# Kernel tuning notes

Hardware: AMD Instinct MI355X
Metric: run time of the kernel (lower is better)

Reference implementation:

```python
import jax, jax.numpy as jnp
import numpy as np

WIN = 256   # win_size
H = 8       # n_heads
D = 256     # feature_dim
DFF = 1024
EPS = 1e-5


def _layer_norm(x, g, b):
    mu = jnp.mean(x, axis=-1, keepdims=True)
    var = jnp.mean((x - mu) ** 2, axis=-1, keepdims=True)
    return (x - mu) * jax.lax.rsqrt(var + EPS) * g + b


def setup_inputs() -> dict:
    key = jax.random.key(0)
    ks = jax.random.split(key, 10)
    B, S = 8, 8192
    s = 0.02
    return {
        "query_em": jax.random.normal(ks[0], (B, S, D), jnp.float32),
        "key_value_em": jax.random.normal(ks[1], (B, S, D), jnp.float32),
        "Wq": jax.random.normal(ks[2], (D, D), jnp.float32) * s,
        "bq": jnp.zeros((D,), jnp.float32),
        "Wk": jax.random.normal(ks[3], (D, D), jnp.float32) * s,
        "bk": jnp.zeros((D,), jnp.float32),
        "Wv": jax.random.normal(ks[4], (D, D), jnp.float32) * s,
        "bv": jnp.zeros((D,), jnp.float32),
        "Wo": jax.random.normal(ks[5], (D, D), jnp.float32) * s,
        "bo": jnp.zeros((D,), jnp.float32),
        "ln1_g": jnp.ones((D,), jnp.float32),
        "ln1_b": jnp.zeros((D,), jnp.float32),
        "W1": jax.random.normal(ks[6], (D, DFF), jnp.float32) * s,
        "b1": jnp.zeros((DFF,), jnp.float32),
        "W2": jax.random.normal(ks[7], (DFF, D), jnp.float32) * s,
        "b2": jnp.zeros((D,), jnp.float32),
        "ln2_g": jnp.ones((D,), jnp.float32),
        "ln2_b": jnp.zeros((D,), jnp.float32),
    }


def reference(query_em, key_value_em, Wq, bq, Wk, bk, Wv, bv, Wo, bo,
              ln1_g, ln1_b, W1, b1, W2, b2, ln2_g, ln2_b):
    B, S, _ = query_em.shape
    nw = S // WIN
    dh = D // H

    # window partition: (B, S, D) -> (B*nw, w, D)
    q_in = query_em.reshape(B * nw, WIN, D)
    kv_in = key_value_em.reshape(B * nw, WIN, D)

    # generate_masks: padding_len == 0 -> all-False (nw, B, w, w) mask,
    # extract the block-diagonal windows, apply per window.
    mask = jnp.zeros((nw, B, WIN, WIN), dtype=bool)
    # reorder to (B*nw, 1, w, w) to broadcast over heads
    mask_bw = jnp.transpose(mask, (1, 0, 2, 3)).reshape(B * nw, 1, WIN, WIN)

    # multi-head cross attention within each window
    Q = (q_in @ Wq + bq).reshape(B * nw, WIN, H, dh)
    K = (kv_in @ Wk + bk).reshape(B * nw, WIN, H, dh)
    V = (kv_in @ Wv + bv).reshape(B * nw, WIN, H, dh)

    scores = jnp.einsum("nqhd,nkhd->nhqk", Q, K) / jnp.sqrt(jnp.float32(dh))
    scores = jnp.where(mask_bw, jnp.finfo(scores.dtype).min, scores)
    attn = jax.nn.softmax(scores, axis=-1)
    ctx = jnp.einsum("nhqk,nkhd->nqhd", attn, V).reshape(B * nw, WIN, D)
    attn_out = ctx @ Wo + bo

    # post-norm transformer encoder layer: residual + LN, FFN + LN
    x = _layer_norm(q_in + attn_out, ln1_g, ln1_b)
    ff = jax.nn.relu(x @ W1 + b1) @ W2 + b2
    y = _layer_norm(x + ff, ln2_g, ln2_b)

    # window merge: (B*nw, w, D) -> (B, S, D); padding_len == 0 so no slice
    return y.reshape(B, S, D)
```

## Files before the change

### kernel.cpp

```cpp
#include <hip/hip_runtime.h>

#define DEV __device__ __forceinline__

typedef short short4v __attribute__((ext_vector_type(4)));
typedef short short8v __attribute__((ext_vector_type(8)));
typedef float float4v __attribute__((ext_vector_type(4)));
typedef unsigned short u16;

DEV unsigned short f2bf(float f) {
  unsigned u = __builtin_bit_cast(unsigned, f);
  u += 0x7fffu + ((u >> 16) & 1u);
  return (unsigned short)(u >> 16);
}
DEV float bf2f(unsigned short h) {
  unsigned u = ((unsigned)h) << 16;
  return __builtin_bit_cast(float, u);
}
DEV float4v mfma32(short8v a, short8v b, float4v c) {
  return __builtin_amdgcn_mfma_f32_16x16x32_bf16(a, b, c, 0, 0, 0);
}
DEV float4v mfma16(short4v a, short4v b, float4v c) {
  return __builtin_amdgcn_mfma_f32_16x16x16bf16_1k(a, b, c, 0, 0, 0);
}
DEV void async16(const void* g, void* l) {
  __builtin_amdgcn_global_load_lds(
      (const __attribute__((address_space(1))) unsigned*)g,
      (__attribute__((address_space(3))) unsigned*)l, 16, 0, 0);
}
DEV short4v cvt4(float4v v) {
  short4v r;
  r[0] = (short)f2bf(v[0]); r[1] = (short)f2bf(v[1]);
  r[2] = (short)f2bf(v[2]); r[3] = (short)f2bf(v[3]);
  return r;
}

__global__ __launch_bounds__(256)
void cvt_in(const float* __restrict__ q, const float* __restrict__ kv,
            u16* __restrict__ qb, u16* __restrict__ kvb) {
  const float* src = blockIdx.y ? kv : q;
  u16* dst = blockIdx.y ? kvb : qb;
  size_t i = ((size_t)blockIdx.x * 256 + threadIdx.x) * 8;
  float4v a = *(const float4v*)(src + i);
  float4v b = *(const float4v*)(src + i + 4);
  short8v o;
  o[0] = (short)f2bf(a[0]); o[1] = (short)f2bf(a[1]);
  o[2] = (short)f2bf(a[2]); o[3] = (short)f2bf(a[3]);
  o[4] = (short)f2bf(b[0]); o[5] = (short)f2bf(b[1]);
  o[6] = (short)f2bf(b[2]); o[7] = (short)f2bf(b[3]);
  *(short8v*)(dst + i) = o;
}

__global__ __launch_bounds__(256)
void cvt_wT(const float* Wq, const float* Wk, const float* Wv, const float* Wo,
            const float* W1, const float* W2,
            u16* Wqt, u16* Wkt, u16* Wvt, u16* Wot, u16* W1t, u16* W2t) {
  __shared__ float ld[64 * 69];
  const float* src; u16* dst; int R, C; bool permk = false;
  switch (blockIdx.y) {
    case 0: src = Wq; dst = Wqt; R = 256;  C = 256;  break;
    case 1: src = Wk; dst = Wkt; R = 256;  C = 256;  break;
    case 2: src = Wv; dst = Wvt; R = 256;  C = 256;  break;
    case 3: src = Wo; dst = Wot; R = 256;  C = 256;  break;
    case 4: src = W1; dst = W1t; R = 256;  C = 1024; break;
    default: src = W2; dst = W2t; R = 1024; C = 256; permk = true; break;
  }
  const int ntile = (R >> 6) * (C >> 6);
  if ((int)blockIdx.x >= ntile) return;
  const int tf = blockIdx.x % (R >> 6);
  const int tn = blockIdx.x / (R >> 6);
  const int r0 = tf << 6, c0 = tn << 6;
  const int tid = threadIdx.x;
  {
    int lr = tid >> 4, lc = (tid & 15) << 2;
    #pragma unroll
    for (int ps = 0; ps < 4; ++ps) {
      int r = ps * 16 + lr;
      float4v v = *(const float4v*)(src + (size_t)(r0 + r) * C + c0 + lc);
      #pragma unroll
      for (int e = 0; e < 4; ++e) ld[r * 69 + lc + e] = v[e];
    }
  }
  __syncthreads();
  {
    int p8 = (tid & 7) << 3;
    #pragma unroll
    for (int ps = 0; ps < 2; ++ps) {
      int n = ps * 32 + (tid >> 3);
      short8v o;
      #pragma unroll
      for (int e = 0; e < 8; ++e) {
        int p = p8 + e;
        int fl = p;
        if (permk) {
          int m = p & 31;
          fl = (p & 32) + 16 * ((m >> 2) & 1) + 4 * (m >> 3) + (m & 3);
        }
        o[e] = (short)f2bf(ld[fl * 69 + n]);
      }
      *(short8v*)(dst + (size_t)(c0 + n) * R + r0 + p8) = o;
    }
  }
}

template<bool RESID>
__global__ __launch_bounds__(256, 2)
void gemm128(const u16* __restrict__ A, const u16* __restrict__ Wt,
             const float* __restrict__ bias, const float* __restrict__ resid,
             u16* __restrict__ out, int M, int N, int K) {
  __shared__ alignas(16) char sm[32768];
  char* sa = sm;
  char* sb = sm + 16384;
  const int tid = threadIdx.x;
  const int w = tid >> 6, lane = tid & 63;
  const int ln15 = lane & 15, gq = lane >> 4;
  const int wr = w >> 1, wc = w & 1;
  const int m0 = blockIdx.x * 128, n0 = blockIdx.y * 128;
  const char* Ab = (const char*)A;
  const char* Wb = (const char*)Wt;
  const int Kb = K * 2;

  float4v acc[4][4] = {};
  const int nk = K >> 6;
  for (int kk = 0; kk < nk; ++kk) {
    #pragma unroll
    for (int p = 0; p < 4; ++p) {
      int L = p * 4096 + w * 1024 + lane * 16;
      int row = L >> 7, colb = L & 127;
      int sw = colb ^ ((row & 7) << 4);
      async16(Ab + (size_t)(m0 + row) * Kb + kk * 128 + sw, sa + p * 4096 + w * 1024);
      async16(Wb + (size_t)(n0 + row) * Kb + kk * 128 + sw, sb + p * 4096 + w * 1024);
    }
    __syncthreads();
    #pragma unroll
    for (int ks = 0; ks < 2; ++ks) {
      short8v af[4], bfr[4];
      #pragma unroll
      for (int mf = 0; mf < 4; ++mf) {
        int r = wr * 64 + mf * 16 + ln15;
        af[mf] = *(const short8v*)(sa + r * 128 + ((ks * 64 + gq * 16) ^ ((r & 7) << 4)));
      }
      #pragma unroll
      for (int nf = 0; nf < 4; ++nf) {
        int r = wc * 64 + nf * 16 + ln15;
        bfr[nf] = *(const short8v*)(sb + r * 128 + ((ks * 64 + gq * 16) ^ ((r & 7) << 4)));
      }
      #pragma unroll
      for (int mf = 0; mf < 4; ++mf)
        #pragma unroll
        for (int nf = 0; nf < 4; ++nf)
          acc[mf][nf] = mfma32(af[mf], bfr[nf], acc[mf][nf]);
    }
    __syncthreads();
  }
  #pragma unroll
  for (int nf = 0; nf < 4; ++nf) {
    int col = n0 + wc * 64 + nf * 16 + ln15;
    float bb = bias[col];
    #pragma unroll
    for (int mf = 0; mf < 4; ++mf) {
      int rb = m0 + wr * 64 + mf * 16 + 4 * gq;
      #pragma unroll
      for (int j = 0; j < 4; ++j) {
        size_t idx = (size_t)(rb + j) * N + col;
        float v = acc[mf][nf][j] + bb;
        if (RESID) v += resid[idx];
        out[idx] = f2bf(v);
      }
    }
  }
}

__global__ __launch_bounds__(256, 2)
void gemm_kv(const u16* __restrict__ A, const u16* __restrict__ Wt,
             const float* __restrict__ bk, const float* __restrict__ bv,
             u16* __restrict__ Kout, u16* __restrict__ Vout) {
  __shared__ alignas(16) char sm[32768];
  char* sa = sm;
  char* sb = sm + 16384;
  const int tid = threadIdx.x;
  const int w = tid >> 6, lane = tid & 63;
  const int ln15 = lane & 15, gq = lane >> 4;
  const int wr = w >> 1, wc = w & 1;
  const int m0 = blockIdx.x * 128, n0 = blockIdx.y * 128;
  const char* Ab = (const char*)A;
  const char* Wb = (const char*)Wt;

  float4v acc[4][4] = {};
  for (int kk = 0; kk < 4; ++kk) {
    #pragma unroll
    for (int p = 0; p < 4; ++p) {
      int L = p * 4096 + w * 1024 + lane * 16;
      int row = L >> 7, colb = L & 127;
      int sw = colb ^ ((row & 7) << 4);
      async16(Ab + (size_t)(m0 + row) * 512 + kk * 128 + sw, sa + p * 4096 + w * 1024);
      async16(Wb + (size_t)(n0 + row) * 512 + kk * 128 + sw, sb + p * 4096 + w * 1024);
    }
    __syncthreads();
    #pragma unroll
    for (int ks = 0; ks < 2; ++ks) {
      short8v af[4], bfr[4];
      #pragma unroll
      for (int mf = 0; mf < 4; ++mf) {
        int r = wr * 64 + mf * 16 + ln15;
        af[mf] = *(const short8v*)(sa + r * 128 + ((ks * 64 + gq * 16) ^ ((r & 7) << 4)));
      }
      #pragma unroll
      for (int nf = 0; nf < 4; ++nf) {
        int r = wc * 64 + nf * 16 + ln15;
        bfr[nf] = *(const short8v*)(sb + r * 128 + ((ks * 64 + gq * 16) ^ ((r & 7) << 4)));
      }
      #pragma unroll
      for (int mf = 0; mf < 4; ++mf)
        #pragma unroll
        for (int nf = 0; nf < 4; ++nf)
          acc[mf][nf] = mfma32(af[mf], bfr[nf], acc[mf][nf]);
    }
    __syncthreads();
  }
  #pragma unroll
  for (int nf = 0; nf < 4; ++nf) {
    int col = n0 + wc * 64 + nf * 16 + ln15;
    const bool isK = col < 256;
    const int c2 = isK ? col : col - 256;
    u16* outp = isK ? Kout : Vout;
    float bb = isK ? bk[c2] : bv[c2];
    #pragma unroll
    for (int mf = 0; mf < 4; ++mf) {
      int rb = m0 + wr * 64 + mf * 16 + 4 * gq;
      #pragma unroll
      for (int j = 0; j < 4; ++j)
        outp[(size_t)(rb + j) * 256 + c2] = f2bf(acc[mf][nf][j] + bb);
    }
  }
}

__global__ __launch_bounds__(256, 2)
void attn_kernel(const u16* __restrict__ Qg, const u16* __restrict__ Kg,
                 const u16* __restrict__ Vg, u16* __restrict__ ctx) {
  __shared__ alignas(16) char vs[256 * 80];
  const int bw = blockIdx.x;
  const int win = bw >> 4, head = (bw >> 1) & 7, qh = bw & 1;
  const int tid = threadIdx.x;
  const int w = tid >> 6, lane = tid & 63;
  const int ln15 = lane & 15, gq = lane >> 4;
  const int tok0 = win << 8;
  const int q0 = qh * 128 + w * 32;

  {
    const u16* src = Vg + (size_t)(tok0 + tid) * 256 + head * 32;
    char* dst = vs + tid * 80;
    #pragma unroll
    for (int i = 0; i < 4; ++i)
      *(short8v*)(dst + i * 16) = *(const short8v*)(src + i * 8);
  }

  short8v qf[2];
  #pragma unroll
  for (int qi = 0; qi < 2; ++qi)
    qf[qi] = *(const short8v*)(Qg + (size_t)(tok0 + q0 + qi * 16 + ln15) * 256 + head * 32 + gq * 8);

  float4v s[16][2];
  #pragma unroll
  for (int kf = 0; kf < 16; ++kf) {
    short8v kfr = *(const short8v*)(Kg + (size_t)(tok0 + kf * 16 + ln15) * 256 + head * 32 + gq * 8);
    float4v z = {0.f, 0.f, 0.f, 0.f};
    s[kf][0] = mfma32(kfr, qf[0], z);
    s[kf][1] = mfma32(kfr, qf[1], z);
  }
  __syncthreads();

  const float KSC = (float)(1.4426950408889634 / 5.656854249492381);
  float rs[2];
  #pragma unroll
  for (int qi = 0; qi < 2; ++qi) {
    float mx = -1e30f;
    #pragma unroll
    for (int kf = 0; kf < 16; ++kf)
      #pragma unroll
      for (int j = 0; j < 4; ++j) mx = fmaxf(mx, s[kf][qi][j]);
    mx = fmaxf(mx, __shfl_xor(mx, 16));
    mx = fmaxf(mx, __shfl_xor(mx, 32));
    float sum = 0.f;
    #pragma unroll
    for (int kf = 0; kf < 16; ++kf)
      #pragma unroll
      for (int j = 0; j < 4; ++j) {
        float p = exp2f((s[kf][qi][j] - mx) * KSC);
        s[kf][qi][j] = p;
        sum += p;
      }
    sum += __shfl_xor(sum, 16);
    sum += __shfl_xor(sum, 32);
    rs[qi] = 1.0f / sum;
  }

  float4v cacc[2][2] = {};
  #pragma unroll
  for (int ks = 0; ks < 16; ++ks) {
    short4v pb[2];
    pb[0] = cvt4(s[ks][0]);
    pb[1] = cvt4(s[ks][1]);
    #pragma unroll
    for (int df = 0; df < 2; ++df) {
      const char* vb = vs + (size_t)(16 * ks + 4 * gq) * 80 + (df * 16 + ln15) * 2;
      short4v va;
      va[0] = *(const short*)(vb);
      va[1] = *(const short*)(vb + 80);
      va[2] = *(const short*)(vb + 160);
      va[3] = *(const short*)(vb + 240);
      cacc[df][0] = mfma16(va, pb[0], cacc[df][0]);
      cacc[df][1] = mfma16(va, pb[1], cacc[df][1]);
    }
  }

  #pragma unroll
  for (int qi = 0; qi < 2; ++qi)
    #pragma unroll
    for (int df = 0; df < 2; ++df) {
      short4v o;
      #pragma unroll
      for (int j = 0; j < 4; ++j) o[j] = (short)f2bf(cacc[df][qi][j] * rs[qi]);
      *(short4v*)(ctx + (size_t)(tok0 + q0 + qi * 16 + ln15) * 256 + head * 32 + df * 16 + 4 * gq) = o;
    }
}

__global__ __launch_bounds__(256, 4)
void ln_rows(u16* __restrict__ x, const float* __restrict__ g, const float* __restrict__ b) {
  int row = blockIdx.x * 4 + (threadIdx.x >> 6);
  int lane = threadIdx.x & 63;
  u16* p = x + (size_t)row * 256 + lane * 4;
  short4v v = *(short4v*)p;
  float f[4];
  #pragma unroll
  for (int i = 0; i < 4; ++i) f[i] = bf2f((unsigned short)v[i]);
  float s = f[0] + f[1] + f[2] + f[3];
  float ss = f[0] * f[0] + f[1] * f[1] + f[2] * f[2] + f[3] * f[3];
  #pragma unroll
  for (int m = 1; m <= 32; m <<= 1) {
    s += __shfl_xor(s, m);
    ss += __shfl_xor(ss, m);
  }
  float mu = s * (1.f / 256.f);
  float var = ss * (1.f / 256.f) - mu * mu;
  float rstd = rsqrtf(var + 1e-5f);
  #pragma unroll
  for (int i = 0; i < 4; ++i) {
    int c = lane * 4 + i;
    float o = (f[i] - mu) * rstd * g[c] + b[c];
    v[i] = (short)f2bf(o);
  }
  *(short4v*)p = v;
}

__global__ __launch_bounds__(512, 2)
void ffn_v6(const u16* __restrict__ X, const u16* __restrict__ W1t,
            const u16* __restrict__ W2tp, const float* __restrict__ b1,
            const float* __restrict__ b2, const float* __restrict__ g2,
            const float* __restrict__ be2, float* __restrict__ out) {
  __shared__ alignas(16) char w1c[2][16384];
  __shared__ alignas(16) char w2c[2][20480];
  __shared__ alignas(16) float b1s[1024];
  const int tid = threadIdx.x;
  const int w = tid >> 6, lane = tid & 63;
  const int ln15 = lane & 15, gq = lane >> 4;
  const int m0 = blockIdx.x * 256;
  const int wrow0 = m0 + w * 32;

  b1s[tid] = b1[tid];
  b1s[tid + 512] = b1[tid + 512];

  short8v xr[2][8];
  #pragma unroll
  for (int ct = 0; ct < 2; ++ct)
    #pragma unroll
    for (int kc = 0; kc < 8; ++kc)
      xr[ct][kc] = *(const short8v*)(X + (size_t)(wrow0 + ct * 16 + ln15) * 256 + kc * 32 + gq * 8);

  float4v ff[2][16] = {};
  short8v w2r[2];

  const char* W1b = (const char*)W1t;
  const char* W2b = (const char*)W2tp;

  #define STAGE_W1(buf, c)                                                     \
    {                                                                          \
      _Pragma("unroll")                                                        \
      for (int p = 0; p < 2; ++p) {                                            \
        int L = p * 8192 + tid * 16;                                           \
        int r = L >> 9, colb = L & 511;                                        \
        async16(W1b + (size_t)((c) * 32 + r) * 512 + (colb ^ ((r & 7) << 4)),  \
                w1c[buf] + L);                                                 \
      }                                                                        \
    }
  #define LOAD_W2(c)                                                           \
    {                                                                          \
      _Pragma("unroll")                                                        \
      for (int p = 0; p < 2; ++p) {                                            \
        int idx = p * 8192 + tid * 16;                                         \
        int n = idx >> 6, off = idx & 63;                                      \
        w2r[p] = *(const short8v*)(W2b + (size_t)n * 2048 + (c) * 64 + off);   \
      }                                                                        \
    }
  #define WRITE_W2(buf)                                                        \
    {                                                                          \
      _Pragma("unroll")                                                        \
      for (int p = 0; p < 2; ++p) {                                            \
        int idx = p * 8192 + tid * 16;                                         \
        int n = idx >> 6, off = idx & 63;                                      \
        *(short8v*)(w2c[buf] + n * 80 + off) = w2r[p];                         \
      }                                                                        \
    }

  STAGE_W1(0, 0);
  LOAD_W2(0);
  WRITE_W2(0);
  __syncthreads();

  #pragma unroll 2
  for (int c = 0; c < 32; ++c) {
    const int buf = c & 1;
    if (c < 31) {
      STAGE_W1(buf ^ 1, c + 1);
      LOAD_W2(c + 1);
    }

    float4v g1[2][2] = {};
    #pragma unroll
    for (int kc = 0; kc < 8; ++kc) {
      #pragma unroll
      for (int ft = 0; ft < 2; ++ft) {
        int r = ft * 16 + ln15;
        short8v a = *(const short8v*)(w1c[buf] + r * 512 +
                                      ((kc * 64 + gq * 16) ^ ((r & 7) << 4)));
        g1[0][ft] = mfma32(a, xr[0][kc], g1[0][ft]);
        g1[1][ft] = mfma32(a, xr[1][kc], g1[1][ft]);
      }
    }
    short8v pa8[2];
    #pragma unroll
    for (int ft = 0; ft < 2; ++ft) {
      float4v bv4 = *(const float4v*)(b1s + c * 32 + ft * 16 + 4 * gq);
      #pragma unroll
      for (int ct = 0; ct < 2; ++ct)
        #pragma unroll
        for (int j = 0; j < 4; ++j) {
          float v = g1[ct][ft][j] + bv4[j];
          v = v > 0.f ? v : 0.f;
          pa8[ct][ft * 4 + j] = (short)f2bf(v);
        }
    }
    #pragma unroll
    for (int nt = 0; nt < 16; ++nt) {
      short8v wb = *(const short8v*)(w2c[buf] + (nt * 16 + ln15) * 80 + gq * 16);
      ff[0][nt] = mfma32(pa8[0], wb, ff[0][nt]);
      ff[1][nt] = mfma32(pa8[1], wb, ff[1][nt]);
    }

    if (c < 31) WRITE_W2(buf ^ 1);
    __syncthreads();
  }

  #pragma unroll
  for (int ct = 0; ct < 2; ++ct)
    #pragma unroll
    for (int j = 0; j < 4; ++j) {
      int r2 = wrow0 + ct * 16 + 4 * gq + j;
      float sum = 0.f, sq = 0.f;
      float vv[16];
      #pragma unroll
      for (int nt = 0; nt < 16; ++nt) {
        int col = nt * 16 + ln15;
        float xv = bf2f(X[(size_t)r2 * 256 + col]);
        float v = ff[ct][nt][j] + b2[col] + xv;
        vv[nt] = v;
        sum += v;
        sq += v * v;
      }
      #pragma unroll
      for (int m = 1; m <= 8; m <<= 1) {
        sum += __shfl_xor(sum, m);
        sq += __shfl_xor(sq, m);
      }
      float mu = sum * (1.f / 256.f);
      float var = sq * (1.f / 256.f) - mu * mu;
      float rstd = rsqrtf(var + 1e-5f);
      #pragma unroll
      for (int nt = 0; nt < 16; ++nt) {
        int col = nt * 16 + ln15;
        out[(size_t)r2 * 256 + col] = (vv[nt] - mu) * rstd * g2[col] + be2[col];
      }
    }
  #undef STAGE_W1
  #undef LOAD_W2
  #undef WRITE_W2
}

extern "C" void kernel_launch(void* const* d_in, const int* in_sizes, int n_in,
                              void* d_out, int out_size, void* d_ws, size_t ws_size,
                              hipStream_t stream) {
  (void)in_sizes; (void)n_in; (void)out_size;
  const float* query = (const float*)d_in[0];
  const float* kv    = (const float*)d_in[1];
  const float* Wqm = (const float*)d_in[2];  const float* bq = (const float*)d_in[3];
  const float* Wkm = (const float*)d_in[4];  const float* bk = (const float*)d_in[5];
  const float* Wvm = (const float*)d_in[6];  const float* bv = (const float*)d_in[7];
  const float* Wom = (const float*)d_in[8];  const float* bo = (const float*)d_in[9];
  const float* ln1g = (const float*)d_in[10]; const float* ln1b = (const float*)d_in[11];
  const float* W1m = (const float*)d_in[12]; const float* b1 = (const float*)d_in[13];
  const float* W2m = (const float*)d_in[14]; const float* b2 = (const float*)d_in[15];
  const float* ln2g = (const float*)d_in[16]; const float* ln2b = (const float*)d_in[17];
  float* out = (float*)d_out;

  char* ws = (char*)d_ws;
  const size_t MB = 1ull << 20;
  if (ws_size < 130 * MB) return;

  u16* qbf  = (u16*)(ws);
  u16* kvbf = (u16*)(ws + 32 * MB);
  u16* Vw   = (u16*)(ws);
  u16* ctxw = (u16*)(ws + 32 * MB);
  u16* Qw   = (u16*)(ws + 64 * MB);
  u16* xw   = (u16*)(ws + 64 * MB);
  u16* Kw   = (u16*)(ws + 96 * MB);
  char* wb = ws + 128 * MB;
  u16* Wqt = (u16*)(wb);
  u16* Wkt = (u16*)(wb + 131072);
  u16* Wvt = (u16*)(wb + 262144);
  u16* Wot = (u16*)(wb + 393216);
  u16* W1t = (u16*)(wb + 524288);
  u16* W2t = (u16*)(wb + 1048576);

  cvt_in<<<dim3(8192, 2), 256, 0, stream>>>(query, kv, qbf, kvbf);
  cvt_wT<<<dim3(64, 6), 256, 0, stream>>>(Wqm, Wkm, Wvm, Wom, W1m, W2m,
                                          Wqt, Wkt, Wvt, Wot, W1t, W2t);
  gemm128<false><<<dim3(512, 2), 256, 0, stream>>>(qbf,  Wqt, bq, nullptr, Qw, 65536, 256, 256);
  gemm_kv<<<dim3(512, 4), 256, 0, stream>>>(kvbf, Wkt, bk, bv, Kw, Vw);
  attn_kernel<<<dim3(4096), 256, 0, stream>>>(Qw, Kw, Vw, ctxw);
  gemm128<true><<<dim3(512, 2), 256, 0, stream>>>(ctxw, Wot, bo, query, xw, 65536, 256, 256);
  ln_rows<<<dim3(16384), 256, 0, stream>>>(xw, ln1g, ln1b);
  ffn_v6<<<dim3(256), 512, 0, stream>>>(xw, W1t, W2t, b1, b2, ln2g, ln2b, out);
}
```

Measured before the change: 346.3 us.

## Use head-major Q/K/V/ctx layout and one block per window-head in attention

The Q, K, V and context tensors are stored head-major ([head][token][32]) instead of token-major, so each attention block reads and writes contiguous 64-byte rows per head. The attention kernel now handles a full window-head per block (2048 blocks) and stages both K and V in LDS once, then runs two query passes per wave. The old split into two blocks per window-head loaded K/V twice. The out-projection GEMM gains an addressing mode that reads A from the head-major ctx layout. This trades fewer blocks and more LDS per block for better coalescing and less redundant K/V traffic.

Measured after the change: 330.4 us. -4.6%, faster.

```diff
diff --git a/kernel.cpp b/kernel.cpp
--- a/kernel.cpp
+++ b/kernel.cpp
@@ -6,6 +6,9 @@
 typedef short short8v __attribute__((ext_vector_type(8)));
 typedef float float4v __attribute__((ext_vector_type(4)));
 typedef unsigned short u16;
+
+#define S32E ((size_t)65536 * 32)
+#define S64B ((size_t)65536 * 64)
 
 DEV unsigned short f2bf(float f) {
   unsigned u = __builtin_bit_cast(unsigned, f);
@@ -102,7 +105,7 @@
   }
 }
 
-template<bool RESID>
+template<bool RESID, bool AHEAD, bool OHEAD>
 __global__ __launch_bounds__(256, 2)
 void gemm128(const u16* __restrict__ A, const u16* __restrict__ Wt,
              const float* __restrict__ bias, const float* __restrict__ resid,
@@ -127,7 +130,13 @@
       int L = p * 4096 + w * 1024 + lane * 16;
       int row = L >> 7, colb = L & 127;
       int sw = colb ^ ((row & 7) << 4);
-      async16(Ab + (size_t)(m0 + row) * Kb + kk * 128 + sw, sa + p * 4096 + w * 1024);
+      if (AHEAD) {
+        int b = kk * 128 + sw;
+        async16(Ab + (size_t)(b >> 6) * S64B + (size_t)(m0 + row) * 64 + (b & 63),
+                sa + p * 4096 + w * 1024);
+      } else {
+        async16(Ab + (size_t)(m0 + row) * Kb + kk * 128 + sw, sa + p * 4096 + w * 1024);
+      }
       async16(Wb + (size_t)(n0 + row) * Kb + kk * 128 + sw, sb + p * 4096 + w * 1024);
     }
     __syncthreads();
@@ -161,10 +170,12 @@
       int rb = m0 + wr * 64 + mf * 16 + 4 * gq;
       #pragma unroll
       for (int j = 0; j < 4; ++j) {
-        size_t idx = (size_t)(rb + j) * N + col;
         float v = acc[mf][nf][j] + bb;
-        if (RESID) v += resid[idx];
-        out[idx] = f2bf(v);
+        if (RESID) v += resid[(size_t)(rb + j) * N + col];
+        if (OHEAD)
+          out[(size_t)(col >> 5) * S32E + (size_t)(rb + j) * 32 + (col & 31)] = f2bf(v);
+        else
+          out[(size_t)(rb + j) * N + col] = f2bf(v);
       }
     }
   }
@@ -221,107 +232,121 @@
   for (int nf = 0; nf < 4; ++nf) {
     int col = n0 + wc * 64 + nf * 16 + ln15;
     const bool isK = col < 256;
-    const int c2 = isK ? col : col - 256;
+    const int c2 = col & 255;
     u16* outp = isK ? Kout : Vout;
     float bb = isK ? bk[c2] : bv[c2];
+    const size_t hb = (size_t)(c2 >> 5) * S32E;
+    const int d = c2 & 31;
     #pragma unroll
     for (int mf = 0; mf < 4; ++mf) {
       int rb = m0 + wr * 64 + mf * 16 + 4 * gq;
       #pragma unroll
       for (int j = 0; j < 4; ++j)
-        outp[(size_t)(rb + j) * 256 + c2] = f2bf(acc[mf][nf][j] + bb);
+        outp[hb + (size_t)(rb + j) * 32 + d] = f2bf(acc[mf][nf][j] + bb);
     }
   }
 }
 
 __global__ __launch_bounds__(256, 2)
-void attn_kernel(const u16* __restrict__ Qg, const u16* __restrict__ Kg,
-                 const u16* __restrict__ Vg, u16* __restrict__ ctx) {
+void attn_v2(const u16* __restrict__ Qg, const u16* __restrict__ Kg,
+             const u16* __restrict__ Vg, u16* __restrict__ ctx) {
+  __shared__ alignas(16) char ks[256 * 80];
   __shared__ alignas(16) char vs[256 * 80];
   const int bw = blockIdx.x;
-  const int win = bw >> 4, head = (bw >> 1) & 7, qh = bw & 1;
+  const int win = bw >> 3, head = bw & 7;
   const int tid = threadIdx.x;
   const int w = tid >> 6, lane = tid & 63;
   const int ln15 = lane & 15, gq = lane >> 4;
   const int tok0 = win << 8;
-  const int q0 = qh * 128 + w * 32;
-
-  {
-    const u16* src = Vg + (size_t)(tok0 + tid) * 256 + head * 32;
-    char* dst = vs + tid * 80;
-    #pragma unroll
-    for (int i = 0; i < 4; ++i)
-      *(short8v*)(dst + i * 16) = *(const short8v*)(src + i * 8);
-  }
-
-  short8v qf[2];
-  #pragma unroll
-  for (int qi = 0; qi < 2; ++qi)
-    qf[qi] = *(const short8v*)(Qg + (size_t)(tok0 + q0 + qi * 16 + ln15) * 256 + head * 32 + gq * 8);
-
-  float4v s[16][2];
-  #pragma unroll
-  for (int kf = 0; kf < 16; ++kf) {
-    short8v kfr = *(const short8v*)(Kg + (size_t)(tok0 + kf * 16 + ln15) * 256 + head * 32 + gq * 8);
-    float4v z = {0.f, 0.f, 0.f, 0.f};
-    s[kf][0] = mfma32(kfr, qf[0], z);
-    s[kf][1] = mfma32(kfr, qf[1], z);
+  const u16* Qh = Qg + head * S32E + (size_t)tok0 * 32;
+  const u16* Kh = Kg + head * S32E + (size_t)tok0 * 32;
+  const u16* Vh = Vg + head * S32E + (size_t)tok0 * 32;
+  u16* Ch = ctx + head * S32E + (size_t)tok0 * 32;
+
+  #pragma unroll
+  for (int i = 0; i < 4; ++i) {
+    int L = i * 4096 + tid * 16;
+    int row = L >> 6, colb = L & 63;
+    short8v kv0 = *(const short8v*)((const char*)Kh + L);
+    short8v vv0 = *(const short8v*)((const char*)Vh + L);
+    *(short8v*)(ks + row * 80 + colb) = kv0;
+    *(short8v*)(vs + row * 80 + colb) = vv0;
   }
   __syncthreads();
 
   const float KSC = (float)(1.4426950408889634 / 5.656854249492381);
-  float rs[2];
-  #pragma unroll
-  for (int qi = 0; qi < 2; ++qi) {
-    float mx = -1e30f;
-    #pragma unroll
-    for (int kf = 0; kf < 16; ++kf)
-      #pragma unroll
-      for (int j = 0; j < 4; ++j) mx = fmaxf(mx, s[kf][qi][j]);
-    mx = fmaxf(mx, __shfl_xor(mx, 16));
-    mx = fmaxf(mx, __shfl_xor(mx, 32));
-    float sum = 0.f;
-    #pragma unroll
-    for (int kf = 0; kf < 16; ++kf)
-      #pragma unroll
-      for (int j = 0; j < 4; ++j) {
-        float p = exp2f((s[kf][qi][j] - mx) * KSC);
-        s[kf][qi][j] = p;
-        sum += p;
-      }
-    sum += __shfl_xor(sum, 16);
-    sum += __shfl_xor(sum, 32);
-    rs[qi] = 1.0f / sum;
-  }
-
-  float4v cacc[2][2] = {};
-  #pragma unroll
-  for (int ks = 0; ks < 16; ++ks) {
-    short4v pb[2];
-    pb[0] = cvt4(s[ks][0]);
-    pb[1] = cvt4(s[ks][1]);
-    #pragma unroll
-    for (int df = 0; df < 2; ++df) {
-      const char* vb = vs + (size_t)(16 * ks + 4 * gq) * 80 + (df * 16 + ln15) * 2;
-      short4v va;
-      va[0] = *(const short*)(vb);
-      va[1] = *(const short*)(vb + 80);
-      va[2] = *(const short*)(vb + 160);
-      va[3] = *(const short*)(vb + 240);
-      cacc[df][0] = mfma16(va, pb[0], cacc[df][0]);
-      cacc[df][1] = mfma16(va, pb[1], cacc[df][1]);
-    }
-  }
-
-  #pragma unroll
-  for (int qi = 0; qi < 2; ++qi)
-    #pragma unroll
-    for (int df = 0; df < 2; ++df) {
-      short4v o;
-      #pragma unroll
-      for (int j = 0; j < 4; ++j) o[j] = (short)f2bf(cacc[df][qi][j] * rs[qi]);
-      *(short4v*)(ctx + (size_t)(tok0 + q0 + qi * 16 + ln15) * 256 + head * 32 + df * 16 + 4 * gq) = o;
-    }
+
+  for (int pass = 0; pass < 2; ++pass) {
+    const int q0 = w * 64 + pass * 32;
+
+    short8v qf[2];
+    #pragma unroll
+    for (int qi = 0; qi < 2; ++qi)
+      qf[qi] = *(const short8v*)(Qh + (size_t)(q0 + qi * 16 + ln15) * 32 + gq * 8);
+
+    float4v s[16][2];
+    #pragma unroll
+    for (int kf = 0; kf < 16; ++kf) {
+      short8v kfr = *(const short8v*)(ks + (16 * kf + ln15) * 80 + gq * 16);
+      float4v z = {0.f, 0.f, 0.f, 0.f};
+      s[kf][0] = mfma32(kfr, qf[0], z);
+      s[kf][1] = mfma32(kfr, qf[1], z);
+    }
+
+    float rs[2];
+    #pragma unroll
+    for (int qi = 0; qi < 2; ++qi) {
+      float mx = -1e30f;
+      #pragma unroll
+      for (int kf = 0; kf < 16; ++kf)
+        #pragma unroll
+        for (int j = 0; j < 4; ++j) mx = fmaxf(mx, s[kf][qi][j]);
+      mx = fmaxf(mx, __shfl_xor(mx, 16));
+      mx = fmaxf(mx, __shfl_xor(mx, 32));
+      float mk = mx * KSC;
+      float sum = 0.f;
+      #pragma unroll
+      for (int kf = 0; kf < 16; ++kf)
+        #pragma unroll
+        for (int j = 0; j < 4; ++j) {
+          float p = exp2f(fmaf(s[kf][qi][j], KSC, -mk));
+          s[kf][qi][j] = p;
+          sum += p;
+        }
+      sum += __shfl_xor(sum, 16);
+      sum += __shfl_xor(sum, 32);
+      rs[qi] = 1.0f / sum;
+    }
+
+    float4v cacc[2][2] = {};
+    #pragma unroll
+    for (int kss = 0; kss < 16; ++kss) {
+      short4v pb[2];
+      pb[0] = cvt4(s[kss][0]);
+      pb[1] = cvt4(s[kss][1]);
+      #pragma unroll
+      for (int df = 0; df < 2; ++df) {
+        const char* vb = vs + (size_t)(16 * kss + 4 * gq) * 80 + (df * 16 + ln15) * 2;
+        short4v va;
+        va[0] = *(const short*)(vb);
+        va[1] = *(const short*)(vb + 80);
+        va[2] = *(const short*)(vb + 160);
+        va[3] = *(const short*)(vb + 240);
+        cacc[df][0] = mfma16(va, pb[0], cacc[df][0]);
+        cacc[df][1] = mfma16(va, pb[1], cacc[df][1]);
+      }
+    }
+
+    #pragma unroll
+    for (int qi = 0; qi < 2; ++qi)
+      #pragma unroll
+      for (int df = 0; df < 2; ++df) {
+        short4v o;
+        #pragma unroll
+        for (int j = 0; j < 4; ++j) o[j] = (short)f2bf(cacc[df][qi][j] * rs[qi]);
+        *(short4v*)(Ch + (size_t)(q0 + qi * 16 + ln15) * 32 + df * 16 + 4 * gq) = o;
+      }
+  }
 }
 
 __global__ __launch_bounds__(256, 4)
@@ -533,10 +558,12 @@
   cvt_in<<<dim3(8192, 2), 256, 0, stream>>>(query, kv, qbf, kvbf);
   cvt_wT<<<dim3(64, 6), 256, 0, stream>>>(Wqm, Wkm, Wvm, Wom, W1m, W2m,
                                           Wqt, Wkt, Wvt, Wot, W1t, W2t);
-  gemm128<false><<<dim3(512, 2), 256, 0, stream>>>(qbf,  Wqt, bq, nullptr, Qw, 65536, 256, 256);
+  gemm128<false, false, true><<<dim3(512, 2), 256, 0, stream>>>(
+      qbf, Wqt, bq, nullptr, Qw, 65536, 256, 256);
   gemm_kv<<<dim3(512, 4), 256, 0, stream>>>(kvbf, Wkt, bk, bv, Kw, Vw);
-  attn_kernel<<<dim3(4096), 256, 0, stream>>>(Qw, Kw, Vw, ctxw);
-  gemm128<true><<<dim3(512, 2), 256, 0, stream>>>(ctxw, Wot, bo, query, xw, 65536, 256, 256);
+  attn_v2<<<dim3(2048), 256, 0, stream>>>(Qw, Kw, Vw, ctxw);
+  gemm128<true, true, false><<<dim3(512, 2), 256, 0, stream>>>(
+      ctxw, Wot, bo, query, xw, 65536, 256, 256);
   ln_rows<<<dim3(16384), 256, 0, stream>>>(xw, ln1g, ln1b);
   ffn_v6<<<dim3(256), 512, 0, stream>>>(xw, W1t, W2t, b1, b2, ln2g, ln2b, out);
 }
```
